# Optimization experiments

Measured on AMD Instinct MI355X. Metric: run time of the kernel, lower is better.

The kernel has to match this reference:

```python
import jax, jax.numpy as jnp
import numpy as np

N = 8192      # n_nodes
F = 512       # input feature dim
MLP = 512     # mlp_channels
C = 256       # output channels
H = 2         # MLP layers
KPI = 10      # power iterations
ALPHA = 0.1   # teleport probability


def setup_inputs() -> dict:
    key = jax.random.key(0)
    ks = jax.random.split(key, 10)
    features = jax.random.normal(ks[0], (N, F), dtype=jnp.float32)
    # dense normalized-adjacency surrogate: nonnegative, rows ~ sum to 1
    fltr = jax.random.uniform(ks[1], (N, N), dtype=jnp.float32) * (2.0 / N)
    s = 1.0 / np.sqrt(F)
    W_mlp0 = jax.random.normal(ks[2], (F, MLP), dtype=jnp.float32) * s
    b_mlp0 = jnp.zeros((MLP,), dtype=jnp.float32)
    W_mlp1 = jax.random.normal(ks[3], (MLP, MLP), dtype=jnp.float32) * (1.0 / np.sqrt(MLP))
    b_mlp1 = jnp.zeros((MLP,), dtype=jnp.float32)
    W_out = jax.random.normal(ks[4], (MLP, C), dtype=jnp.float32) * (1.0 / np.sqrt(MLP))
    b_out = jnp.zeros((C,), dtype=jnp.float32)
    return {"features": features, "fltr": fltr,
            "W_mlp0": W_mlp0, "b_mlp0": b_mlp0,
            "W_mlp1": W_mlp1, "b_mlp1": b_mlp1,
            "W_out": W_out, "b_out": b_out}


def reference(features, fltr, W_mlp0, b_mlp0, W_mlp1, b_mlp1, W_out, b_out):
    # MLP stage: per layer -> X = relu( A @ (X W + b) )   (dropout_rate = 0)
    x = features
    for W, b in ((W_mlp0, b_mlp0), (W_mlp1, b_mlp1)):
        x = jnp.matmul(fltr, jnp.matmul(x, W) + b)  # [N, MLP]
        x = jax.nn.relu(x)
    # output projection
    z0 = jnp.matmul(x, W_out) + b_out  # [N, C]
    # K-step APPNP power iteration: Z <- (1-alpha) A Z + alpha Z0
    def step(z, _):
        z = (1.0 - ALPHA) * jnp.matmul(fltr, z) + ALPHA * z0
        return z, None
    z, _ = jax.lax.scan(step, z0, None, length=KPI)
    return jax.nn.softmax(z, axis=-1)
```

## Files before the change

### kernel.cpp

```cpp
#include <hip/hip_runtime.h>

typedef unsigned short u16;
typedef __attribute__((ext_vector_type(8))) short bf16x8;
typedef __attribute__((ext_vector_type(4))) float f32x4;

__device__ __forceinline__ float bf2f(u16 u) {
    union { unsigned i; float f; } v; v.i = ((unsigned)u) << 16; return v.f;
}
__device__ __forceinline__ u16 f2bf(float f) {
    union { float f; unsigned i; } v; v.f = f;
    unsigned r = v.i + 0x7FFFu + ((v.i >> 16) & 1u);
    return (u16)(r >> 16);
}

#define GL2LDS(g, l) __builtin_amdgcn_global_load_lds(                         \
    (const __attribute__((address_space(1))) void*)(g),                        \
    (__attribute__((address_space(3))) void*)(l), 16, 0, 0)

template<int EPI, int AFP32>
__global__ __launch_bounds__(256, 4)
void gemm_bt(const void* __restrict__ Ap, int lda,
             const u16* __restrict__ Bt, int ldb,
             int KB,
             void* __restrict__ outp,
             const void* __restrict__ aux,
             int ldout, int NC)
{
    __shared__ u16 aL[128 * 64];
    __shared__ u16 bL[128 * 64];

    const int t = threadIdx.x;
    const int wid = t >> 6, lane = t & 63;
    const int quad = lane >> 4, l15 = lane & 15;
    const int m0 = blockIdx.x * 128, n0 = blockIdx.y * 128;
    const int sk = blockIdx.z;
    const int k0 = sk * KB * 64;

    f32x4 acc[4][4];
    const f32x4 z4 = {0.f, 0.f, 0.f, 0.f};
#pragma unroll
    for (int i = 0; i < 4; ++i)
#pragma unroll
        for (int j = 0; j < 4; ++j) acc[i][j] = z4;

    const int wm = (wid >> 1) * 64, wn = (wid & 1) * 64;

    if (AFP32 == 0) {
        const char* pa[4]; const char* pb[4]; int lo[4];
#pragma unroll
        for (int i = 0; i < 4; ++i) {
            int flat = i * 4096 + wid * 1024 + lane * 16;
            int row  = flat >> 7;
            int col  = flat & 127;
            pa[i] = (const char*)Ap + ((size_t)(m0 + row) * lda + k0) * 2 + col;
            pb[i] = (const char*)Bt + ((size_t)(n0 + row) * ldb + k0) * 2 + col;
            lo[i] = i * 4096 + wid * 1024;
        }
        for (int kb = 0; kb < KB; ++kb) {
#pragma unroll
            for (int i = 0; i < 4; ++i) GL2LDS(pa[i], (char*)aL + lo[i]);
#pragma unroll
            for (int i = 0; i < 4; ++i) GL2LDS(pb[i], (char*)bL + lo[i]);
#pragma unroll
            for (int i = 0; i < 4; ++i) { pa[i] += 128; pb[i] += 128; }
            __syncthreads();
#pragma unroll
            for (int ks = 0; ks < 2; ++ks) {
                const int cr = (ks * 4 + quad) * 8;
                bf16x8 av[4], bv[4];
#pragma unroll
                for (int mi = 0; mi < 4; ++mi)
                    av[mi] = *(const bf16x8*)(aL + (wm + mi * 16 + l15) * 64 + cr);
#pragma unroll
                for (int ni = 0; ni < 4; ++ni)
                    bv[ni] = *(const bf16x8*)(bL + (wn + ni * 16 + l15) * 64 + cr);
#pragma unroll
                for (int mi = 0; mi < 4; ++mi)
#pragma unroll
                    for (int ni = 0; ni < 4; ++ni)
                        acc[mi][ni] = __builtin_amdgcn_mfma_f32_16x16x32_bf16(
                            av[mi], bv[ni], acc[mi][ni], 0, 0, 0);
            }
            __syncthreads();
        }
    } else {
        for (int kb = 0; kb < KB; ++kb) {
            const int kbase = k0 + kb * 64;
#pragma unroll
            for (int i = 0; i < 4; ++i) {
                int flat = i * 4096 + t * 16;
                int row  = flat >> 7;
                int col  = (flat & 127) >> 1;
                bf16x8 v = *(const bf16x8*)(Bt + (size_t)(n0 + row) * ldb + kbase + col);
                *(bf16x8*)(bL + row * 64 + col) = v;
            }
            const float* Af = (const float*)Ap;
#pragma unroll
            for (int j = 0; j < 8; ++j) {
                int f = j * 256 + t;
                int r = f >> 4, c = (f & 15) * 4;
                float4 v = *(const float4*)(Af + (size_t)(m0 + r) * lda + kbase + c);
                ushort4 o;
                o.x = f2bf(v.x); o.y = f2bf(v.y);
                o.z = f2bf(v.z); o.w = f2bf(v.w);
                *(ushort4*)(aL + r * 64 + c) = o;
            }
            __syncthreads();
#pragma unroll
            for (int ks = 0; ks < 2; ++ks) {
                const int cr = (ks * 4 + quad) * 8;
                bf16x8 av[4], bv[4];
#pragma unroll
                for (int mi = 0; mi < 4; ++mi)
                    av[mi] = *(const bf16x8*)(aL + (wm + mi * 16 + l15) * 64 + cr);
#pragma unroll
                for (int ni = 0; ni < 4; ++ni)
                    bv[ni] = *(const bf16x8*)(bL + (wn + ni * 16 + l15) * 64 + cr);
#pragma unroll
                for (int mi = 0; mi < 4; ++mi)
#pragma unroll
                    for (int ni = 0; ni < 4; ++ni)
                        acc[mi][ni] = __builtin_amdgcn_mfma_f32_16x16x32_bf16(
                            av[mi], bv[ni], acc[mi][ni], 0, 0, 0);
            }
            __syncthreads();
        }
    }

    if (EPI == 0) {
#pragma unroll
        for (int ni = 0; ni < 4; ++ni) {
            int n = n0 + wn + ni * 16 + l15;
            float bvv = ((const float*)aux)[n];
            u16* ob = (u16*)outp + (size_t)n * ldout;
#pragma unroll
            for (int mi = 0; mi < 4; ++mi) {
                int m = m0 + wm + mi * 16 + quad * 4;
                ushort4 o;
                o.x = f2bf(acc[mi][ni][0] + bvv);
                o.y = f2bf(acc[mi][ni][1] + bvv);
                o.z = f2bf(acc[mi][ni][2] + bvv);
                o.w = f2bf(acc[mi][ni][3] + bvv);
                *(ushort4*)(ob + m) = o;
            }
        }
    } else if (EPI == 2) {
#pragma unroll
        for (int ni = 0; ni < 4; ++ni) {
            int n = n0 + wn + ni * 16 + l15;
            float* ob = (float*)outp + ((size_t)(sk * NC + n)) * 8192;
#pragma unroll
            for (int mi = 0; mi < 4; ++mi) {
                int m = m0 + wm + mi * 16 + quad * 4;
                float4 o;
                o.x = acc[mi][ni][0]; o.y = acc[mi][ni][1];
                o.z = acc[mi][ni][2]; o.w = acc[mi][ni][3];
                *(float4*)(ob + m) = o;
            }
        }
    } else if (EPI == 3) {
#pragma unroll
        for (int ni = 0; ni < 4; ++ni) {
            int n = n0 + wn + ni * 16 + l15;
            const u16* zrow = (const u16*)aux + (size_t)n * 8192;
            u16* ob = (u16*)outp + (size_t)n * ldout;
#pragma unroll
            for (int mi = 0; mi < 4; ++mi) {
                int m = m0 + wm + mi * 16 + quad * 4;
                ushort4 z0 = *(const ushort4*)(zrow + m);
                ushort4 o;
                o.x = f2bf(0.9f * acc[mi][ni][0] + 0.1f * bf2f(z0.x));
                o.y = f2bf(0.9f * acc[mi][ni][1] + 0.1f * bf2f(z0.y));
                o.z = f2bf(0.9f * acc[mi][ni][2] + 0.1f * bf2f(z0.z));
                o.w = f2bf(0.9f * acc[mi][ni][3] + 0.1f * bf2f(z0.w));
                *(ushort4*)(ob + m) = o;
            }
        }
    } else {
        u16* ob = (u16*)outp;
#pragma unroll
        for (int mi = 0; mi < 4; ++mi) {
            int m = m0 + wm + mi * 16 + quad * 4;
#pragma unroll
            for (int ni = 0; ni < 4; ++ni) {
                int n = n0 + wn + ni * 16 + l15;
#pragma unroll
                for (int r = 0; r < 4; ++r)
                    ob[(size_t)(m + r) * ldout + n] = f2bf(fmaxf(acc[mi][ni][r], 0.0f));
            }
        }
    }
}

__global__ __launch_bounds__(256)
void cvt_f2b_k(const float* __restrict__ in, u16* __restrict__ out, long n4)
{
    long i = (long)blockIdx.x * 256 + threadIdx.x;
    long stride = (long)gridDim.x * 256;
    for (; i < n4; i += stride) {
        float4 v = ((const float4*)in)[i];
        ushort4 o;
        o.x = f2bf(v.x); o.y = f2bf(v.y); o.z = f2bf(v.z); o.w = f2bf(v.w);
        ((ushort4*)out)[i] = o;
    }
}

__global__ __launch_bounds__(256)
void transpose_cvt_k(const float* __restrict__ in, u16* __restrict__ out,
                     int R, int C)
{
    __shared__ u16 tile[32][33];
    int tx = threadIdx.x, ty = threadIdx.y;
    int x = blockIdx.x * 32 + tx;
    int y0 = blockIdx.y * 32 + ty;
#pragma unroll
    for (int j = 0; j < 32; j += 8)
        tile[ty + j][tx] = f2bf(in[(size_t)(y0 + j) * C + x]);
    __syncthreads();
    int x2 = blockIdx.y * 32 + tx;
    int y2 = blockIdx.x * 32 + ty;
#pragma unroll
    for (int j = 0; j < 32; j += 8)
        out[(size_t)(y2 + j) * R + x2] = tile[tx][ty + j];
}

__global__ __launch_bounds__(256)
void combine_mlp_k(const float* __restrict__ part, u16* __restrict__ y)
{
    __shared__ u16 L[64][68];
    const int t = threadIdx.x;
    const int mb = blockIdx.x * 64;
    const int nb = blockIdx.y * 64;
    const size_t S = (size_t)512 * 8192;
#pragma unroll
    for (int i = 0; i < 4; ++i) {
        int flat = i * 256 + t;
        int nl = flat >> 4;
        int mq = flat & 15;
        const float* p0 = part + (size_t)(nb + nl) * 8192 + mb + mq * 4;
        float4 a = *(const float4*)p0;
        float4 b = *(const float4*)(p0 + S);
        ushort4 o;
        o.x = f2bf(fmaxf(a.x + b.x, 0.f));
        o.y = f2bf(fmaxf(a.y + b.y, 0.f));
        o.z = f2bf(fmaxf(a.z + b.z, 0.f));
        o.w = f2bf(fmaxf(a.w + b.w, 0.f));
        *(ushort4*)&L[nl][mq * 4] = o;
    }
    __syncthreads();
#pragma unroll
    for (int i = 0; i < 4; ++i) {
        int flat = i * 256 + t;
        int ml  = flat >> 4;
        int nl4 = (flat & 15) * 4;
        ushort4 o;
        o.x = L[nl4 + 0][ml]; o.y = L[nl4 + 1][ml];
        o.z = L[nl4 + 2][ml]; o.w = L[nl4 + 3][ml];
        *(ushort4*)(y + (size_t)(mb + ml) * 512 + nb + nl4) = o;
    }
}

__global__ __launch_bounds__(256)
void combine_iter_k(const float* __restrict__ part, const u16* __restrict__ z0T,
                    u16* __restrict__ zT)
{
    const size_t S = (size_t)256 * 8192;
    size_t e = ((size_t)blockIdx.x * 256 + threadIdx.x) * 4;
    float4 a = *(const float4*)(part + e);
    float4 b = *(const float4*)(part + S + e);
    float4 c = *(const float4*)(part + 2 * S + e);
    float4 d = *(const float4*)(part + 3 * S + e);
    ushort4 z0 = *(const ushort4*)(z0T + e);
    ushort4 o;
    o.x = f2bf(0.9f * (a.x + b.x + c.x + d.x) + 0.1f * bf2f(z0.x));
    o.y = f2bf(0.9f * (a.y + b.y + c.y + d.y) + 0.1f * bf2f(z0.y));
    o.z = f2bf(0.9f * (a.z + b.z + c.z + d.z) + 0.1f * bf2f(z0.z));
    o.w = f2bf(0.9f * (a.w + b.w + c.w + d.w) + 0.1f * bf2f(z0.w));
    *(ushort4*)(zT + e) = o;
}

__global__ __launch_bounds__(256)
void softmax_k(const u16* __restrict__ zT, float* __restrict__ out)
{
    __shared__ u16 L[64][260];
    const int t = threadIdx.x;
    const int m0 = blockIdx.x * 64;
    const int tx = t & 15, ty = t >> 4;
#pragma unroll
    for (int i = 0; i < 16; ++i) {
        int n = i * 16 + ty;
        ushort4 v = *(const ushort4*)(zT + (size_t)n * 8192 + m0 + tx * 4);
        L[tx * 4 + 0][n] = v.x; L[tx * 4 + 1][n] = v.y;
        L[tx * 4 + 2][n] = v.z; L[tx * 4 + 3][n] = v.w;
    }
    __syncthreads();
    const int wid = t >> 6, lane = t & 63;
    for (int r = 0; r < 16; ++r) {
        int mm = wid * 16 + r;
        ushort4 u = *(const ushort4*)(&L[mm][lane * 4]);
        float f0 = bf2f(u.x), f1 = bf2f(u.y), f2 = bf2f(u.z), f3 = bf2f(u.w);
        float mx = fmaxf(fmaxf(f0, f1), fmaxf(f2, f3));
#pragma unroll
        for (int off = 32; off > 0; off >>= 1) mx = fmaxf(mx, __shfl_xor(mx, off));
        float e0 = __expf(f0 - mx), e1 = __expf(f1 - mx);
        float e2 = __expf(f2 - mx), e3 = __expf(f3 - mx);
        float s = e0 + e1 + e2 + e3;
#pragma unroll
        for (int off = 32; off > 0; off >>= 1) s += __shfl_xor(s, off);
        float inv = 1.0f / s;
        float4 o;
        o.x = e0 * inv; o.y = e1 * inv; o.z = e2 * inv; o.w = e3 * inv;
        *(float4*)(out + (size_t)(m0 + mm) * 256 + lane * 4) = o;
    }
}

extern "C" void kernel_launch(void* const* d_in, const int* in_sizes, int n_in,
                              void* d_out, int out_size, void* d_ws, size_t ws_size,
                              hipStream_t stream)
{
    const float* features = (const float*)d_in[0];
    const float* fltr     = (const float*)d_in[1];
    const float* W0       = (const float*)d_in[2];
    const float* b0       = (const float*)d_in[3];
    const float* W1       = (const float*)d_in[4];
    const float* b1       = (const float*)d_in[5];
    const float* Wo       = (const float*)d_in[6];
    const float* bo       = (const float*)d_in[7];

    dim3 tb(32, 8);

    char* p = (char*)d_ws;
    u16* fB  = (u16*)p;  p += (size_t)8192 * 512 * 2;
    u16* W0T = (u16*)p;  p += (size_t)512 * 512 * 2;
    u16* W1T = (u16*)p;  p += (size_t)512 * 512 * 2;
    u16* WoT = (u16*)p;  p += (size_t)256 * 512 * 2;
    u16* z0T = (u16*)p;  p += (size_t)256 * 8192 * 2;
    u16* zA  = (u16*)p;  p += (size_t)256 * 8192 * 2;
    u16* zB  = (u16*)p;  p += (size_t)256 * 8192 * 2;
    u16* tT  = (u16*)p;  p += (size_t)512 * 8192 * 2;
    u16* y   = (u16*)p;  p += (size_t)8192 * 512 * 2;
    float* part = (float*)p; p += (size_t)2 * 512 * 8192 * 4;
    size_t base_need = (size_t)(p - (char*)d_ws);
    u16* fltrB = (u16*)p;
    size_t full_need = base_need + (size_t)8192 * 8192 * 2;

    if (ws_size >= full_need) {
        cvt_f2b_k<<<2048, 256, 0, stream>>>(fltr, fltrB, (long)8192 * 8192 / 4);
        cvt_f2b_k<<<512, 256, 0, stream>>>(features, fB, (long)8192 * 512 / 4);
        transpose_cvt_k<<<dim3(16, 16), tb, 0, stream>>>(W0, W0T, 512, 512);
        transpose_cvt_k<<<dim3(16, 16), tb, 0, stream>>>(W1, W1T, 512, 512);
        transpose_cvt_k<<<dim3(8, 16),  tb, 0, stream>>>(Wo, WoT, 512, 256);

        gemm_bt<0, 0><<<dim3(64, 4), 256, 0, stream>>>(fB, 512, W0T, 512, 8,
                                                       tT, b0, 8192, 0);
        gemm_bt<2, 0><<<dim3(64, 4, 2), 256, 0, stream>>>(fltrB, 8192, tT, 8192,
                                                          64, part, nullptr, 0, 512);
        combine_mlp_k<<<dim3(128, 8), 256, 0, stream>>>(part, y);
        gemm_bt<0, 0><<<dim3(64, 4), 256, 0, stream>>>(y, 512, W1T, 512, 8,
                                                       tT, b1, 8192, 0);
        gemm_bt<2, 0><<<dim3(64, 4, 2), 256, 0, stream>>>(fltrB, 8192, tT, 8192,
                                                          64, part, nullptr, 0, 512);
        combine_mlp_k<<<dim3(128, 8), 256, 0, stream>>>(part, y);
        gemm_bt<0, 0><<<dim3(64, 2), 256, 0, stream>>>(y, 512, WoT, 512, 8,
                                                       z0T, bo, 8192, 0);
        const u16* src = z0T;
        for (int it = 0; it < 10; ++it) {
            u16* dst = (it & 1) ? zB : zA;
            gemm_bt<2, 0><<<dim3(64, 2, 4), 256, 0, stream>>>(fltrB, 8192, src,
                                                              8192, 32, part,
                                                              nullptr, 0, 256);
            combine_iter_k<<<2048, 256, 0, stream>>>(part, z0T, dst);
            src = dst;
        }
        softmax_k<<<128, 256, 0, stream>>>(src, (float*)d_out);
    } else if (ws_size >= base_need) {
        cvt_f2b_k<<<512, 256, 0, stream>>>(features, fB, (long)8192 * 512 / 4);
        transpose_cvt_k<<<dim3(16, 16), tb, 0, stream>>>(W0, W0T, 512, 512);
        transpose_cvt_k<<<dim3(16, 16), tb, 0, stream>>>(W1, W1T, 512, 512);
        transpose_cvt_k<<<dim3(8, 16),  tb, 0, stream>>>(Wo, WoT, 512, 256);

        gemm_bt<0, 0><<<dim3(64, 4), 256, 0, stream>>>(fB, 512, W0T, 512, 8,
                                                       tT, b0, 8192, 0);
        gemm_bt<2, 1><<<dim3(64, 4, 2), 256, 0, stream>>>(fltr, 8192, tT, 8192,
                                                          64, part, nullptr, 0, 512);
        combine_mlp_k<<<dim3(128, 8), 256, 0, stream>>>(part, y);
        gemm_bt<0, 0><<<dim3(64, 4), 256, 0, stream>>>(y, 512, W1T, 512, 8,
                                                       tT, b1, 8192, 0);
        gemm_bt<2, 1><<<dim3(64, 4, 2), 256, 0, stream>>>(fltr, 8192, tT, 8192,
                                                          64, part, nullptr, 0, 512);
        combine_mlp_k<<<dim3(128, 8), 256, 0, stream>>>(part, y);
        gemm_bt<0, 0><<<dim3(64, 2), 256, 0, stream>>>(y, 512, WoT, 512, 8,
                                                       z0T, bo, 8192, 0);
        const u16* src = z0T;
        for (int it = 0; it < 10; ++it) {
            u16* dst = (it & 1) ? zB : zA;
            gemm_bt<2, 1><<<dim3(64, 2, 4), 256, 0, stream>>>(fltr, 8192, src,
                                                              8192, 32, part,
                                                              nullptr, 0, 256);
            combine_iter_k<<<2048, 256, 0, stream>>>(part, z0T, dst);
            src = dst;
        }
        softmax_k<<<128, 256, 0, stream>>>(src, (float*)d_out);
    } else {
        char* w = (char*)d_ws;
        u16* fW0T = (u16*)w;  w += (size_t)512 * 512 * 2;
        u16* fW1T = (u16*)w;  w += (size_t)512 * 512 * 2;
        u16* fWoT = (u16*)w;  w += (size_t)256 * 512 * 2;
        u16* fz0T = (u16*)w;  w += (size_t)256 * 8192 * 2;
        char* rb = w;
        u16* ftT = (u16*)rb;
        u16* fy  = (u16*)(rb + (size_t)512 * 8192 * 2);
        u16* fzA = (u16*)rb;
        u16* fzB = (u16*)(rb + (size_t)256 * 8192 * 2);

        transpose_cvt_k<<<dim3(16, 16), tb, 0, stream>>>(W0, fW0T, 512, 512);
        transpose_cvt_k<<<dim3(16, 16), tb, 0, stream>>>(W1, fW1T, 512, 512);
        transpose_cvt_k<<<dim3(8, 16),  tb, 0, stream>>>(Wo, fWoT, 512, 256);
        gemm_bt<0, 1><<<dim3(64, 4), 256, 0, stream>>>(features, 512, fW0T, 512, 8,
                                                       ftT, b0, 8192, 0);
        gemm_bt<1, 1><<<dim3(64, 4), 256, 0, stream>>>(fltr, 8192, ftT, 8192, 128,
                                                       fy, nullptr, 512, 0);
        gemm_bt<0, 0><<<dim3(64, 4), 256, 0, stream>>>(fy, 512, fW1T, 512, 8,
                                                       ftT, b1, 8192, 0);
        gemm_bt<1, 1><<<dim3(64, 4), 256, 0, stream>>>(fltr, 8192, ftT, 8192, 128,
                                                       fy, nullptr, 512, 0);
        gemm_bt<0, 0><<<dim3(64, 2), 256, 0, stream>>>(fy, 512, fWoT, 512, 8,
                                                       fz0T, bo, 8192, 0);
        const u16* src = fz0T;
        for (int it = 0; it < 10; ++it) {
            u16* dst = (it & 1) ? fzB : fzA;
            gemm_bt<3, 1><<<dim3(64, 2), 256, 0, stream>>>(fltr, 8192, src, 8192,
                                                           128, dst, fz0T, 8192, 0);
            src = dst;
        }
        softmax_k<<<128, 256, 0, stream>>>(src, (float*)d_out);
    }
}
```

Before: 1.269 ms.

## XOR-swizzle GEMM LDS tiles and deepen split-K across all GEMMs

Applies an XOR swizzle to the bf16 LDS tile layout, on both the global-to-LDS source columns and the fragment reads, to avoid LDS bank conflicts. Split-K depth is raised for the adjacency GEMMs (2→4 for the MLP layers, 4→8 for the power iterations). The small weight GEMMs now also use split-K, followed by a new bias-adding combine kernel. This is meant to fill more CUs on an MI355X-sized grid, at the cost of more fp32 partial-sum traffic, extra combine launches and a larger workspace.

```diff
diff --git a/kernel.cpp b/kernel.cpp
--- a/kernel.cpp
+++ b/kernel.cpp
@@ -31,7 +31,7 @@
 
     const int t = threadIdx.x;
     const int wid = t >> 6, lane = t & 63;
-    const int quad = lane >> 4, l15 = lane & 15;
+    const int quad = lane >> 4, l15 = lane & 15, l7 = lane & 7;
     const int m0 = blockIdx.x * 128, n0 = blockIdx.y * 128;
     const int sk = blockIdx.z;
     const int k0 = sk * KB * 64;
@@ -51,9 +51,9 @@
         for (int i = 0; i < 4; ++i) {
             int flat = i * 4096 + wid * 1024 + lane * 16;
             int row  = flat >> 7;
-            int col  = flat & 127;
-            pa[i] = (const char*)Ap + ((size_t)(m0 + row) * lda + k0) * 2 + col;
-            pb[i] = (const char*)Bt + ((size_t)(n0 + row) * ldb + k0) * 2 + col;
+            int csrc = ((flat >> 4) & 7) ^ (row & 7);
+            pa[i] = (const char*)Ap + ((size_t)(m0 + row) * lda + k0) * 2 + csrc * 16;
+            pb[i] = (const char*)Bt + ((size_t)(n0 + row) * ldb + k0) * 2 + csrc * 16;
             lo[i] = i * 4096 + wid * 1024;
         }
         for (int kb = 0; kb < KB; ++kb) {
@@ -66,7 +66,7 @@
             __syncthreads();
 #pragma unroll
             for (int ks = 0; ks < 2; ++ks) {
-                const int cr = (ks * 4 + quad) * 8;
+                const int cr = ((ks * 4 + quad) ^ l7) * 8;
                 bf16x8 av[4], bv[4];
 #pragma unroll
                 for (int mi = 0; mi < 4; ++mi)
@@ -224,6 +224,28 @@
         out[(size_t)(y2 + j) * R + x2] = tile[tx][ty + j];
 }
 
+template<int S>
+__global__ __launch_bounds__(256)
+void combine_bias_k(const float* __restrict__ part, const float* __restrict__ bias,
+                    u16* __restrict__ out, long NROW)
+{
+    const size_t Sz = (size_t)NROW * 8192;
+    size_t e = ((size_t)blockIdx.x * 256 + threadIdx.x) * 4;
+    int n = (int)(e >> 13);
+    float b = bias[n];
+    float4 s = *(const float4*)(part + e);
+#pragma unroll
+    for (int i = 1; i < S; ++i) {
+        float4 v = *(const float4*)(part + (size_t)i * Sz + e);
+        s.x += v.x; s.y += v.y; s.z += v.z; s.w += v.w;
+    }
+    ushort4 o;
+    o.x = f2bf(s.x + b); o.y = f2bf(s.y + b);
+    o.z = f2bf(s.z + b); o.w = f2bf(s.w + b);
+    *(ushort4*)(out + e) = o;
+}
+
+template<int S>
 __global__ __launch_bounds__(256)
 void combine_mlp_k(const float* __restrict__ part, u16* __restrict__ y)
 {
@@ -231,7 +253,7 @@
     const int t = threadIdx.x;
     const int mb = blockIdx.x * 64;
     const int nb = blockIdx.y * 64;
-    const size_t S = (size_t)512 * 8192;
+    const size_t Sz = (size_t)512 * 8192;
 #pragma unroll
     for (int i = 0; i < 4; ++i) {
         int flat = i * 256 + t;
@@ -239,12 +261,14 @@
         int mq = flat & 15;
         const float* p0 = part + (size_t)(nb + nl) * 8192 + mb + mq * 4;
         float4 a = *(const float4*)p0;
-        float4 b = *(const float4*)(p0 + S);
+#pragma unroll
+        for (int s = 1; s < S; ++s) {
+            float4 v = *(const float4*)(p0 + (size_t)s * Sz);
+            a.x += v.x; a.y += v.y; a.z += v.z; a.w += v.w;
+        }
         ushort4 o;
-        o.x = f2bf(fmaxf(a.x + b.x, 0.f));
-        o.y = f2bf(fmaxf(a.y + b.y, 0.f));
-        o.z = f2bf(fmaxf(a.z + b.z, 0.f));
-        o.w = f2bf(fmaxf(a.w + b.w, 0.f));
+        o.x = f2bf(fmaxf(a.x, 0.f)); o.y = f2bf(fmaxf(a.y, 0.f));
+        o.z = f2bf(fmaxf(a.z, 0.f)); o.w = f2bf(fmaxf(a.w, 0.f));
         *(ushort4*)&L[nl][mq * 4] = o;
     }
     __syncthreads();
@@ -260,22 +284,25 @@
     }
 }
 
+template<int S>
 __global__ __launch_bounds__(256)
 void combine_iter_k(const float* __restrict__ part, const u16* __restrict__ z0T,
                     u16* __restrict__ zT)
 {
-    const size_t S = (size_t)256 * 8192;
+    const size_t Sz = (size_t)256 * 8192;
     size_t e = ((size_t)blockIdx.x * 256 + threadIdx.x) * 4;
     float4 a = *(const float4*)(part + e);
-    float4 b = *(const float4*)(part + S + e);
-    float4 c = *(const float4*)(part + 2 * S + e);
-    float4 d = *(const float4*)(part + 3 * S + e);
+#pragma unroll
+    for (int s = 1; s < S; ++s) {
+        float4 v = *(const float4*)(part + (size_t)s * Sz + e);
+        a.x += v.x; a.y += v.y; a.z += v.z; a.w += v.w;
+    }
     ushort4 z0 = *(const ushort4*)(z0T + e);
     ushort4 o;
-    o.x = f2bf(0.9f * (a.x + b.x + c.x + d.x) + 0.1f * bf2f(z0.x));
-    o.y = f2bf(0.9f * (a.y + b.y + c.y + d.y) + 0.1f * bf2f(z0.y));
-    o.z = f2bf(0.9f * (a.z + b.z + c.z + d.z) + 0.1f * bf2f(z0.z));
-    o.w = f2bf(0.9f * (a.w + b.w + c.w + d.w) + 0.1f * bf2f(z0.w));
+    o.x = f2bf(0.9f * a.x + 0.1f * bf2f(z0.x));
+    o.y = f2bf(0.9f * a.y + 0.1f * bf2f(z0.y));
+    o.z = f2bf(0.9f * a.z + 0.1f * bf2f(z0.z));
+    o.w = f2bf(0.9f * a.w + 0.1f * bf2f(z0.w));
     *(ushort4*)(zT + e) = o;
 }
 
@@ -339,7 +366,7 @@
     u16* zB  = (u16*)p;  p += (size_t)256 * 8192 * 2;
     u16* tT  = (u16*)p;  p += (size_t)512 * 8192 * 2;
     u16* y   = (u16*)p;  p += (size_t)8192 * 512 * 2;
-    float* part = (float*)p; p += (size_t)2 * 512 * 8192 * 4;
+    float* part = (float*)p; p += (size_t)4 * 512 * 8192 * 4;
     size_t base_need = (size_t)(p - (char*)d_ws);
     u16* fltrB = (u16*)p;
     size_t full_need = base_need + (size_t)8192 * 8192 * 2;
@@ -351,25 +378,28 @@
         transpose_cvt_k<<<dim3(16, 16), tb, 0, stream>>>(W1, W1T, 512, 512);
         transpose_cvt_k<<<dim3(8, 16),  tb, 0, stream>>>(Wo, WoT, 512, 256);
 
-        gemm_bt<0, 0><<<dim3(64, 4), 256, 0, stream>>>(fB, 512, W0T, 512, 8,
-                                                       tT, b0, 8192, 0);
-        gemm_bt<2, 0><<<dim3(64, 4, 2), 256, 0, stream>>>(fltrB, 8192, tT, 8192,
-                                                          64, part, nullptr, 0, 512);
-        combine_mlp_k<<<dim3(128, 8), 256, 0, stream>>>(part, y);
-        gemm_bt<0, 0><<<dim3(64, 4), 256, 0, stream>>>(y, 512, W1T, 512, 8,
-                                                       tT, b1, 8192, 0);
-        gemm_bt<2, 0><<<dim3(64, 4, 2), 256, 0, stream>>>(fltrB, 8192, tT, 8192,
-                                                          64, part, nullptr, 0, 512);
-        combine_mlp_k<<<dim3(128, 8), 256, 0, stream>>>(part, y);
-        gemm_bt<0, 0><<<dim3(64, 2), 256, 0, stream>>>(y, 512, WoT, 512, 8,
-                                                       z0T, bo, 8192, 0);
+        gemm_bt<2, 0><<<dim3(64, 4, 2), 256, 0, stream>>>(fB, 512, W0T, 512, 4,
+                                                          part, nullptr, 0, 512);
+        combine_bias_k<2><<<4096, 256, 0, stream>>>(part, b0, tT, 512);
+        gemm_bt<2, 0><<<dim3(64, 4, 4), 256, 0, stream>>>(fltrB, 8192, tT, 8192,
+                                                          32, part, nullptr, 0, 512);
+        combine_mlp_k<4><<<dim3(128, 8), 256, 0, stream>>>(part, y);
+        gemm_bt<2, 0><<<dim3(64, 4, 2), 256, 0, stream>>>(y, 512, W1T, 512, 4,
+                                                          part, nullptr, 0, 512);
+        combine_bias_k<2><<<4096, 256, 0, stream>>>(part, b1, tT, 512);
+        gemm_bt<2, 0><<<dim3(64, 4, 4), 256, 0, stream>>>(fltrB, 8192, tT, 8192,
+                                                          32, part, nullptr, 0, 512);
+        combine_mlp_k<4><<<dim3(128, 8), 256, 0, stream>>>(part, y);
+        gemm_bt<2, 0><<<dim3(64, 2, 4), 256, 0, stream>>>(y, 512, WoT, 512, 2,
+                                                          part, nullptr, 0, 256);
+        combine_bias_k<4><<<2048, 256, 0, stream>>>(part, bo, z0T, 256);
         const u16* src = z0T;
         for (int it = 0; it < 10; ++it) {
             u16* dst = (it & 1) ? zB : zA;
-            gemm_bt<2, 0><<<dim3(64, 2, 4), 256, 0, stream>>>(fltrB, 8192, src,
-                                                              8192, 32, part,
+            gemm_bt<2, 0><<<dim3(64, 2, 8), 256, 0, stream>>>(fltrB, 8192, src,
+                                                              8192, 16, part,
                                                               nullptr, 0, 256);
-            combine_iter_k<<<2048, 256, 0, stream>>>(part, z0T, dst);
+            combine_iter_k<8><<<2048, 256, 0, stream>>>(part, z0T, dst);
             src = dst;
         }
         softmax_k<<<128, 256, 0, stream>>>(src, (float*)d_out);
@@ -379,25 +409,28 @@
         transpose_cvt_k<<<dim3(16, 16), tb, 0, stream>>>(W1, W1T, 512, 512);
         transpose_cvt_k<<<dim3(8, 16),  tb, 0, stream>>>(Wo, WoT, 512, 256);
 
-        gemm_bt<0, 0><<<dim3(64, 4), 256, 0, stream>>>(fB, 512, W0T, 512, 8,
-                                                       tT, b0, 8192, 0);
-        gemm_bt<2, 1><<<dim3(64, 4, 2), 256, 0, stream>>>(fltr, 8192, tT, 8192,
-                                                          64, part, nullptr, 0, 512);
-        combine_mlp_k<<<dim3(128, 8), 256, 0, stream>>>(part, y);
-        gemm_bt<0, 0><<<dim3(64, 4), 256, 0, stream>>>(y, 512, W1T, 512, 8,
-                                                       tT, b1, 8192, 0);
-        gemm_bt<2, 1><<<dim3(64, 4, 2), 256, 0, stream>>>(fltr, 8192, tT, 8192,
-                                                          64, part, nullptr, 0, 512);
-        combine_mlp_k<<<dim3(128, 8), 256, 0, stream>>>(part, y);
-        gemm_bt<0, 0><<<dim3(64, 2), 256, 0, stream>>>(y, 512, WoT, 512, 8,
-                                                       z0T, bo, 8192, 0);
+        gemm_bt<2, 0><<<dim3(64, 4, 2), 256, 0, stream>>>(fB, 512, W0T, 512, 4,
+                                                          part, nullptr, 0, 512);
+        combine_bias_k<2><<<4096, 256, 0, stream>>>(part, b0, tT, 512);
+        gemm_bt<2, 1><<<dim3(64, 4, 4), 256, 0, stream>>>(fltr, 8192, tT, 8192,
+                                                          32, part, nullptr, 0, 512);
+        combine_mlp_k<4><<<dim3(128, 8), 256, 0, stream>>>(part, y);
+        gemm_bt<2, 0><<<dim3(64, 4, 2), 256, 0, stream>>>(y, 512, W1T, 512, 4,
+                                                          part, nullptr, 0, 512);
+        combine_bias_k<2><<<4096, 256, 0, stream>>>(part, b1, tT, 512);
+        gemm_bt<2, 1><<<dim3(64, 4, 4), 256, 0, stream>>>(fltr, 8192, tT, 8192,
+                                                          32, part, nullptr, 0, 512);
+        combine_mlp_k<4><<<dim3(128, 8), 256, 0, stream>>>(part, y);
+        gemm_bt<2, 0><<<dim3(64, 2, 4), 256, 0, stream>>>(y, 512, WoT, 512, 2,
+                                                          part, nullptr, 0, 256);
+        combine_bias_k<4><<<2048, 256, 0, stream>>>(part, bo, z0T, 256);
         const u16* src = z0T;
         for (int it = 0; it < 10; ++it) {
             u16* dst = (it & 1) ? zB : zA;
-            gemm_bt<2, 1><<<dim3(64, 2, 4), 256, 0, stream>>>(fltr, 8192, src,
-                                                              8192, 32, part,
+            gemm_bt<2, 1><<<dim3(64, 2, 8), 256, 0, stream>>>(fltr, 8192, src,
+                                                              8192, 16, part,
                                                               nullptr, 0, 256);
-            combine_iter_k<<<2048, 256, 0, stream>>>(part, z0T, dst);
+            combine_iter_k<8><<<2048, 256, 0, stream>>>(part, z0T, dst);
             src = dst;
         }
         softmax_k<<<128, 256, 0, stream>>>(src, (float*)d_out);
```

Measured after the change: 1.214 ms. 4.3% less time.
